# Kernel optimization log

Measured on AMD Instinct MI355X. Metric: run time of the kernel, lower is better.

## Reference

```python
import jax, jax.numpy as jnp
import numpy as np

DIM = 1024
HID = 2048
E = 8
K = 2
EPS = 1e-9


def setup_inputs() -> dict:
    key = jax.random.key(0)
    ks = jax.random.split(key, 6)
    scale = 0.02
    return {
        "x": jax.random.normal(ks[0], (4, 2048, DIM), jnp.float32),
        "gate_w": jax.random.normal(ks[1], (DIM, E), jnp.float32) * scale,
        "gate_b": jnp.zeros((E,), jnp.float32),
        # stacked expert weights: leading dim = expert index
        "w1": jax.random.normal(ks[2], (E, DIM, HID), jnp.float32) * scale,
        "b1": jnp.zeros((E, HID), jnp.float32),
        "w2": jax.random.normal(ks[3], (E, DIM, HID), jnp.float32) * scale,
        "b2": jnp.zeros((E, HID), jnp.float32),
        "w3": jax.random.normal(ks[4], (E, HID, DIM), jnp.float32) * scale,
        "b3": jnp.zeros((E, DIM), jnp.float32),
    }


def reference(x, gate_w, gate_b, w1, b1, w2, b2, w3, b3):
    # x: (b, s, d)
    logits = x @ gate_w + gate_b                      # (b, s, E)
    scores = jax.nn.softmax(logits, axis=-1)
    topk_scores, topk_idx = jax.lax.top_k(scores, K)  # (b, s, K)

    usage = scores.mean(axis=(0, 1))                  # (E,)
    load_balance_loss = jnp.sum(usage * jnp.log(usage + EPS))

    # per-expert combine weight: score if expert in top-k else 0  -> (b, s, E)
    onehot = jax.nn.one_hot(topk_idx, E, dtype=x.dtype)            # (b, s, K, E)
    combine = jnp.sum(topk_scores[..., None] * onehot, axis=2)     # (b, s, E)

    out = jnp.zeros_like(x)
    for e in range(E):  # small fixed loop over experts
        gate = jax.nn.sigmoid(x @ w2[e] + b2[e])      # (b, s, H)
        h = (x @ w1[e] + b1[e]) * gate                # SwiGLU hidden
        out = out + combine[..., e:e + 1] * (h @ w3[e] + b3[e])
    return out, load_balance_loss
```

## Files before the change

kernel.cpp:

```cpp
#include <hip/hip_runtime.h>
#include <hip/hip_bf16.h>
#include <math.h>

#define N_TOK 8192
#define DIM   1024
#define HID   2048
#define NE    8
#define NT1   16
#define NT2   32
#define NB1   16
#define NB2   4
#define MAXT  72
#define PANEL1_SH ((size_t)(128 * 256 * 8))
#define PANEL3_SH ((size_t)(256 * 256 * 8))
#define XBLK_SH   ((size_t)(128 * 128 * 8))
#define HBLK_SH   ((size_t)(256 * 128 * 8))

typedef __attribute__((ext_vector_type(8))) short short8;
typedef __attribute__((ext_vector_type(4))) float f32x4;
typedef unsigned short us;

__device__ __forceinline__ us f2bf(float f) {
    unsigned int u = __builtin_bit_cast(unsigned int, f);
    unsigned int r = (u + 0x7fffu + ((u >> 16) & 1u)) >> 16;
    return (us)r;
}

__device__ __forceinline__ void gl_lds16(const us* g, us* l) {
    __builtin_amdgcn_global_load_lds(
        (const __attribute__((address_space(1))) void*)g,
        (__attribute__((address_space(3))) void*)l, 16, 0, 0);
}

#define VMW4 asm volatile("s_waitcnt vmcnt(4)" ::: "memory")
#define VMW0 asm volatile("s_waitcnt vmcnt(0)" ::: "memory")
#define BARM asm volatile("s_barrier" ::: "memory")
#define PRIO1 __builtin_amdgcn_s_setprio(1)
#define PRIO0 __builtin_amdgcn_s_setprio(0)

__global__ __launch_bounds__(256) void gate_compute(
    const float* __restrict__ x, const float* __restrict__ gw, const float* __restrict__ gb,
    int* __restrict__ sel, float2* __restrict__ wpair, float* __restrict__ usage_part)
{
    const int lane = threadIdx.x & 63;
    const int tok = blockIdx.x * 4 + (threadIdx.x >> 6);

    __shared__ float su[NE];
    if (threadIdx.x < NE) su[threadIdx.x] = 0.f;
    __syncthreads();

    float acc[NE];
#pragma unroll
    for (int e = 0; e < NE; e++) acc[e] = 0.f;

    const float* xr = x + (size_t)tok * DIM;
    for (int d = lane; d < DIM; d += 64) {
        float xv = xr[d];
        const float4* g4 = (const float4*)(gw + (size_t)d * NE);
        float4 ga = g4[0], gc = g4[1];
        acc[0] = fmaf(xv, ga.x, acc[0]);
        acc[1] = fmaf(xv, ga.y, acc[1]);
        acc[2] = fmaf(xv, ga.z, acc[2]);
        acc[3] = fmaf(xv, ga.w, acc[3]);
        acc[4] = fmaf(xv, gc.x, acc[4]);
        acc[5] = fmaf(xv, gc.y, acc[5]);
        acc[6] = fmaf(xv, gc.z, acc[6]);
        acc[7] = fmaf(xv, gc.w, acc[7]);
    }
#pragma unroll
    for (int e = 0; e < NE; e++) {
#pragma unroll
        for (int off = 32; off > 0; off >>= 1)
            acc[e] += __shfl_xor(acc[e], off);
    }

    if (lane == 0) {
        float lg[NE], p[NE];
        float mx = -1e30f;
#pragma unroll
        for (int e = 0; e < NE; e++) { lg[e] = acc[e] + gb[e]; mx = fmaxf(mx, lg[e]); }
        float s = 0.f;
#pragma unroll
        for (int e = 0; e < NE; e++) { p[e] = __expf(lg[e] - mx); s += p[e]; }
        float inv = 1.f / s;
#pragma unroll
        for (int e = 0; e < NE; e++) p[e] *= inv;
#pragma unroll
        for (int e = 0; e < NE; e++) atomicAdd(&su[e], p[e]);

        int e1 = 0; float v1 = p[0];
#pragma unroll
        for (int e = 1; e < NE; e++) if (p[e] > v1) { v1 = p[e]; e1 = e; }
        int e2 = -1; float v2 = -1e30f;
#pragma unroll
        for (int e = 0; e < NE; e++) if (e != e1 && p[e] > v2) { v2 = p[e]; e2 = e; }

        sel[tok] = e1 | (e2 << 4);
        wpair[tok] = make_float2(v1, v2);
    }
    __syncthreads();
    if (threadIdx.x < NE) usage_part[blockIdx.x * NE + threadIdx.x] = su[threadIdx.x];
}

__global__ __launch_bounds__(256) void scan_kernel(
    const int* __restrict__ sel, const float2* __restrict__ wpair,
    int* __restrict__ counts, int* __restrict__ lists, float* __restrict__ wlist)
{
    const int e = blockIdx.x;
    const int t = threadIdx.x;
    const int base_tok = t * 32;

    unsigned selm = 0, km = 0;
#pragma unroll
    for (int i = 0; i < 32; i++) {
        int s = sel[base_tok + i];
        int e1 = s & 15, e2 = (s >> 4) & 15;
        if (e1 == e) selm |= (1u << i);
        else if (e2 == e) { selm |= (1u << i); km |= (1u << i); }
    }
    const int myc = __popc(selm);

    __shared__ int tot[256];
    tot[t] = myc;
    __syncthreads();
#pragma unroll
    for (int d = 1; d < 256; d <<= 1) {
        int v = (t >= d) ? tot[t - d] : 0;
        __syncthreads();
        tot[t] += v;
        __syncthreads();
    }
    int pos = tot[t] - myc;
    if (t == 255) counts[e] = tot[255];

    for (int i = 0; i < 32; i++) {
        if (selm & (1u << i)) {
            int tok = base_tok + i;
            int k = (km >> i) & 1;
            lists[e * N_TOK + pos] = tok * 2 + k;
            float2 wp = wpair[tok];
            wlist[e * N_TOK + pos] = k ? wp.y : wp.x;
            pos++;
        }
    }
}

__global__ __launch_bounds__(256) void usage_reduce(
    const float* __restrict__ part, float* __restrict__ usage)
{
    const int t = threadIdx.x;
    const int e = t & 7, chunk = t >> 3;
    float s = 0.f;
    for (int b = chunk; b < 2048; b += 32) s += part[b * NE + e];
    __shared__ float red[256];
    red[t] = s;
    __syncthreads();
#pragma unroll
    for (int step = 128; step >= 8; step >>= 1) {
        if (t < step) red[t] += red[t + step];
        __syncthreads();
    }
    if (t < NE) usage[t] = red[t];
}

__global__ void loss_kernel(const float* __restrict__ usage, float* __restrict__ out_loss)
{
    if (threadIdx.x == 0) {
        float l = 0.f;
        for (int e = 0; e < NE; e++) {
            float u = usage[e] / (float)N_TOK;
            l += u * logf(u + 1e-9f);
        }
        *out_loss = l;
    }
}

__global__ void prefix_kernel(const int* __restrict__ counts,
                              int* __restrict__ base_exact, int* __restrict__ ntiles,
                              int* __restrict__ tmap_e, int* __restrict__ tmap_m0)
{
    if (threadIdx.x == 0) {
        int bx = 0, nt = 0;
        for (int e = 0; e < NE; e++) {
            base_exact[e] = bx;
            for (int m0 = 0; m0 < counts[e]; m0 += 256) {
                tmap_e[nt] = e; tmap_m0[nt] = m0; nt++;
            }
            bx += counts[e];
        }
        ntiles[0] = nt;
    }
}

__global__ __launch_bounds__(256) void inv_kernel(
    const int* __restrict__ counts, const int* __restrict__ lists,
    const int* __restrict__ base_exact, int* __restrict__ inv)
{
    const int e = blockIdx.y;
    const int idx = blockIdx.x * 256 + threadIdx.x;
    if (idx < counts[e]) inv[lists[e * N_TOK + idx]] = base_exact[e] + idx;
}

__global__ __launch_bounds__(256) void xgather_kernel(
    const float* __restrict__ x,
    const int* __restrict__ counts, const int* __restrict__ lists,
    const int* __restrict__ base_exact,
    us* __restrict__ Xg)
{
    __shared__ int toks[128];
    __shared__ int bexs[NE], cnts[NE];
    const int t = threadIdx.x;
    if (t < NE) { bexs[t] = base_exact[t]; cnts[t] = counts[t]; }
    __syncthreads();
    if (t < 128) {
        int gpos = blockIdx.x * 128 + t;
        int e = 0;
#pragma unroll
        for (int k = 1; k < NE; k++) if (gpos >= bexs[k]) e = k;
        int idx = gpos - bexs[e];
        int tok = (idx < cnts[e]) ? (lists[e * N_TOK + idx] >> 1) : 0;
        toks[t] = tok;
    }
    __syncthreads();

    us* op = Xg + (size_t)blockIdx.x * XBLK_SH;
    const int rr = t & 127;
    const int ch = t >> 7;
    const int tok = toks[rr];
#pragma unroll
    for (int it = 0; it < 64; it++) {
        int c = it * 2 + ch;
        const float4* src = (const float4*)(x + (size_t)tok * DIM + c * 8);
        float4 a = src[0], b = src[1];
        short8 v;
        v[0] = (short)f2bf(a.x); v[1] = (short)f2bf(a.y);
        v[2] = (short)f2bf(a.z); v[3] = (short)f2bf(a.w);
        v[4] = (short)f2bf(b.x); v[5] = (short)f2bf(b.y);
        v[6] = (short)f2bf(b.z); v[7] = (short)f2bf(b.w);
        *(short8*)(op + (size_t)(c * 128 + rr) * 8) = v;
    }
}

__global__ __launch_bounds__(256) void wswz12_kernel(
    const float* __restrict__ w1, const float* __restrict__ w2, us* __restrict__ out)
{
    const int e = blockIdx.z, nbx = blockIdx.y, gs = blockIdx.x;
    us* op = out + ((size_t)e * NB1 + nbx) * PANEL1_SH + (size_t)gs * 8 * 256 * 8;
    const float* w1e = w1 + (size_t)e * DIM * HID;
    const float* w2e = w2 + (size_t)e * DIM * HID;
    const int t = threadIdx.x;
#pragma unroll
    for (int it = 0; it < 8; it++) {
        int idx = it * 256 + t;
        int g = idx >> 8, row = idx & 255;
        int col = nbx * 128 + (row & 127);
        const float* src = (row < 128 ? w1e : w2e) + (size_t)((gs * 8 + g) * 8) * HID + col;
        short8 v;
#pragma unroll
        for (int s = 0; s < 8; s++) v[s] = (short)f2bf(src[(size_t)s * HID]);
        *(short8*)(op + (size_t)idx * 8) = v;
    }
}

__global__ __launch_bounds__(256) void wswz3_kernel(
    const float* __restrict__ w3, us* __restrict__ out)
{
    const int e = blockIdx.z, nbx = blockIdx.y, gs = blockIdx.x;
    us* op = out + ((size_t)e * NB2 + nbx) * PANEL3_SH + (size_t)gs * 8 * 256 * 8;
    const float* w3e = w3 + (size_t)e * HID * DIM;
    const int t = threadIdx.x;
#pragma unroll
    for (int it = 0; it < 8; it++) {
        int idx = it * 256 + t;
        int g = idx >> 8, row = idx & 255;
        int col = nbx * 256 + row;
        const float* src = w3e + (size_t)((gs * 8 + g) * 8) * DIM + col;
        short8 v;
#pragma unroll
        for (int s = 0; s < 8; s++) v[s] = (short)f2bf(src[(size_t)s * DIM]);
        *(short8*)(op + (size_t)idx * 8) = v;
    }
}

#define ABUF(b) ((us*)(SM + (b)*32768))
#define BBUF(b) ((us*)(SM + 65536 + (b)*32768))

#define AF_READ(b, h) do {                                               \
    _Pragma("unroll")                                                    \
    for (int mi = 0; mi < 8; mi++)                                       \
        af[mi] = *(const short8*)(ABUF(b) + ((h)*1024 + kc*256 + Mw + mi*16 + fr)*8); \
} while (0)
#define BF_READ4(b, h) do {                                              \
    _Pragma("unroll")                                                    \
    for (int j = 0; j < 4; j++)                                          \
        bfv[j] = *(const short8*)(BBUF(b) + ((h)*1024 + kc*256 + Nw + j*16 + fr)*8); \
} while (0)
#define CLUST4 do {                                                      \
    PRIO1;                                                               \
    _Pragma("unroll")                                                    \
    for (int j = 0; j < 4; j++) {                                        \
        _Pragma("unroll")                                                \
        for (int mi = 0; mi < 8; mi++)                                   \
            acc[mi][j] = __builtin_amdgcn_mfma_f32_16x16x32_bf16(        \
                af[mi], bfv[j], acc[mi][j], 0, 0, 0);                    \
    }                                                                    \
    PRIO0;                                                               \
} while (0)

__global__ __launch_bounds__(512, 2) void ffn1_mfma_kernel(
    const us* __restrict__ Xg, const us* __restrict__ W12sw,
    const float* __restrict__ b1, const float* __restrict__ b2,
    const int* __restrict__ counts, const int* __restrict__ base_exact,
    const int* __restrict__ ntiles, const int* __restrict__ tmap_e, const int* __restrict__ tmap_m0,
    us* __restrict__ Hsw)
{
    const int hw = blockIdx.x;
    const int ix = hw >> 3;
    const int nbx = ((hw & 7) << 1) | (ix & 1);
    const int by  = ix >> 1;
    if (by >= ntiles[0]) return;
    const int e  = tmap_e[by];
    const int m0 = tmap_m0[by];
    const int cnt = counts[e];
    const int bex = base_exact[e];

    __shared__ __align__(16) unsigned char SM[132096];

    const int t = threadIdx.x;
    const int lane = t & 63, wv = t >> 6;
    const int wr = wv >> 2, wc = wv & 3;
    const int Mw = wr * 128, Nw = wc * 64;
    const int fr = lane & 15, kc = lane >> 4;

    float bb[4];
    {
        const float* bsrc = (wc < 2) ? b1 : b2;
#pragma unroll
        for (int ni = 0; ni < 4; ni++)
            bb[ni] = bsrc[e * HID + nbx * 128 + (wc & 1) * 64 + ni * 16 + fr];
    }
    __syncthreads();

    const int c0 = wv * 128 + lane;
    const int c1 = c0 + 64;
    const int RA0 = min(bex + m0 + (c0 & 255), N_TOK * 2 - 1);
    const int RA1 = min(bex + m0 + (c1 & 255), N_TOK * 2 - 1);
    const us* ApA = Xg + (size_t)(RA0 >> 7) * XBLK_SH + (size_t)(c0 >> 8) * 1024 + (RA0 & 127) * 8;
    const us* ApB = Xg + (size_t)(RA1 >> 7) * XBLK_SH + (size_t)(c1 >> 8) * 1024 + (RA1 & 127) * 8;
    const us* Wp = W12sw + ((size_t)e * NB1 + nbx) * PANEL1_SH;
    const int dbase = wv * 128 * 8;

    f32x4 acc[8][4];
    const f32x4 fz = {0.f, 0.f, 0.f, 0.f};
#pragma unroll
    for (int i = 0; i < 8; i++)
#pragma unroll
        for (int j = 0; j < 4; j++) acc[i][j] = fz;

    #define STAGE_A(b, tile, h) do {                                             \
        gl_lds16(ApA + (size_t)((tile)*8 + (h)*4) * 1024, ABUF(b) + ((h)*1024)*8 + dbase); \
        gl_lds16(ApB + (size_t)((tile)*8 + (h)*4) * 1024, ABUF(b) + ((h)*1024 + 64)*8 + dbase); \
    } while (0)
    #define STAGE_B(b, tile, h) do {                                             \
        const us* s_ = Wp + ((size_t)(tile)*2048 + (h)*1024) * 8;                \
        gl_lds16(s_ + (size_t)c0 * 8, BBUF(b) + ((h)*1024)*8 + dbase);           \
        gl_lds16(s_ + (size_t)c1 * 8, BBUF(b) + ((h)*1024 + 64)*8 + dbase);      \
    } while (0)

    short8 af[8], bfv[4];

    STAGE_A(0, 0, 0); STAGE_B(0, 0, 0); STAGE_A(0, 0, 1); STAGE_B(0, 0, 1);
    VMW4; BARM;

    for (int tl = 0; tl < NT1; ++tl) {
        const int b = tl & 1, nb = b ^ 1;
        const bool more = (tl + 1 < NT1);
        AF_READ(b, 0); BF_READ4(b, 0);
        if (more) { STAGE_A(nb, tl + 1, 0); STAGE_B(nb, tl + 1, 0); VMW4; } else { VMW0; }
        BARM; CLUST4; BARM;
        AF_READ(b, 1); BF_READ4(b, 1);
        if (more) { STAGE_A(nb, tl + 1, 1); STAGE_B(nb, tl + 1, 1); VMW4; }
        BARM; CLUST4; BARM;
    }
    #undef STAGE_A
    #undef STAGE_B

    float* G = (float*)SM;
    if (wc >= 2) {
        const int cp = wc - 2;
#pragma unroll
        for (int ni = 0; ni < 4; ni++) {
            int c2 = cp * 64 + ni * 16 + fr;
#pragma unroll
            for (int mi = 0; mi < 8; mi++) {
#pragma unroll
                for (int j = 0; j < 4; j++) {
                    int m = mi * 16 + kc * 4 + j;
                    float g = 1.f / (1.f + __expf(-(acc[mi][ni][j] + bb[ni])));
                    G[(wr * 128 + c2) * 129 + m] = g;
                }
            }
        }
    }
    __syncthreads();
    if (wc < 2) {
#pragma unroll
        for (int ni = 0; ni < 4; ni++) {
            int c2 = wc * 64 + ni * 16 + fr;
            int ch = nbx * 128 + c2;
            size_t cb = (size_t)(ch >> 3) * 128 * 8 + (ch & 7);
#pragma unroll
            for (int mi = 0; mi < 8; mi++) {
#pragma unroll
                for (int j = 0; j < 4; j++) {
                    int m = mi * 16 + kc * 4 + j;
                    int rl = wr * 128 + m;
                    if (m0 + rl >= cnt) continue;
                    float h = (acc[mi][ni][j] + bb[ni]) * G[(wr * 128 + c2) * 129 + m];
                    int R = bex + m0 + rl;
                    Hsw[(size_t)(R >> 7) * HBLK_SH + cb + (size_t)(R & 127) * 8] = f2bf(h);
                }
            }
        }
    }
}

__global__ __launch_bounds__(512, 2) void ffn2_mfma_kernel(
    const us* __restrict__ Hsw, const us* __restrict__ W3sw, const float* __restrict__ b3,
    const int* __restrict__ counts, const int* __restrict__ base_exact,
    const int* __restrict__ ntiles, const int* __restrict__ tmap_e, const int* __restrict__ tmap_m0,
    const float* __restrict__ wts,
    float* __restrict__ P, int pan0)
{
    const int hw = blockIdx.x;
    const int xcd = hw & 7;
    const int ix = hw >> 3;
    const int pn = xcd >> 2;
    const int by = (ix << 2) | (xcd & 3);
    if (by >= ntiles[0]) return;
    const int e  = tmap_e[by];
    const int m0 = tmap_m0[by];
    const int cnt = counts[e];
    const int bex = base_exact[e];
    const int nbx = pan0 + pn;

    __shared__ __align__(16) unsigned char SM[132096];
    float* rowwt = (float*)(SM + 131072);

    const int t = threadIdx.x;
    if (t < 256) {
        int idx = m0 + t;
        rowwt[t] = (idx < cnt) ? wts[e * N_TOK + idx] : 0.f;
    }

    const int lane = t & 63, wv = t >> 6;
    const int wr = wv >> 2, wc = wv & 3;
    const int Mw = wr * 128, Nw = wc * 64;
    const int fr = lane & 15, kc = lane >> 4;

    float bb3[4];
#pragma unroll
    for (int ni = 0; ni < 4; ni++)
        bb3[ni] = b3[e * DIM + nbx * 256 + wc * 64 + ni * 16 + fr];
    __syncthreads();

    const int c0 = wv * 128 + lane;
    const int c1 = c0 + 64;
    const int RA0 = min(bex + m0 + (c0 & 255), N_TOK * 2 - 1);
    const int RA1 = min(bex + m0 + (c1 & 255), N_TOK * 2 - 1);
    const us* HpA = Hsw + (size_t)(RA0 >> 7) * HBLK_SH + (size_t)(c0 >> 8) * 1024 + (RA0 & 127) * 8;
    const us* HpB = Hsw + (size_t)(RA1 >> 7) * HBLK_SH + (size_t)(c1 >> 8) * 1024 + (RA1 & 127) * 8;
    const us* Wp = W3sw + ((size_t)e * NB2 + nbx) * PANEL3_SH;
    const int dbase = wv * 128 * 8;

    f32x4 acc[8][4];
    const f32x4 fz = {0.f, 0.f, 0.f, 0.f};
#pragma unroll
    for (int i = 0; i < 8; i++)
#pragma unroll
        for (int j = 0; j < 4; j++) acc[i][j] = fz;

    #define STAGE_A2(b, tile, h) do {                                            \
        gl_lds16(HpA + (size_t)((tile)*8 + (h)*4) * 1024, ABUF(b) + ((h)*1024)*8 + dbase); \
        gl_lds16(HpB + (size_t)((tile)*8 + (h)*4) * 1024, ABUF(b) + ((h)*1024 + 64)*8 + dbase); \
    } while (0)
    #define STAGE_B2(b, tile, h) do {                                            \
        const us* s_ = Wp + ((size_t)(tile)*2048 + (h)*1024) * 8;                \
        gl_lds16(s_ + (size_t)c0 * 8, BBUF(b) + ((h)*1024)*8 + dbase);           \
        gl_lds16(s_ + (size_t)c1 * 8, BBUF(b) + ((h)*1024 + 64)*8 + dbase);      \
    } while (0)

    short8 af[8], bfv[4];

    STAGE_A2(0, 0, 0); STAGE_B2(0, 0, 0); STAGE_A2(0, 0, 1); STAGE_B2(0, 0, 1);
    VMW4; BARM;

    for (int tl = 0; tl < NT2; ++tl) {
        const int b = tl & 1, nb = b ^ 1;
        const bool more = (tl + 1 < NT2);
        AF_READ(b, 0); BF_READ4(b, 0);
        if (more) { STAGE_A2(nb, tl + 1, 0); STAGE_B2(nb, tl + 1, 0); VMW4; } else { VMW0; }
        BARM; CLUST4; BARM;
        AF_READ(b, 1); BF_READ4(b, 1);
        if (more) { STAGE_A2(nb, tl + 1, 1); STAGE_B2(nb, tl + 1, 1); VMW4; }
        BARM; CLUST4; BARM;
    }
    #undef STAGE_A2
    #undef STAGE_B2

#pragma unroll
    for (int ni = 0; ni < 4; ni++) {
        int cp = pn * 256 + wc * 64 + ni * 16 + fr;
#pragma unroll
        for (int mi = 0; mi < 8; mi++) {
#pragma unroll
            for (int j = 0; j < 4; j++) {
                int rl = wr * 128 + mi * 16 + kc * 4 + j;
                if (m0 + rl >= cnt) continue;
                float v = (acc[mi][ni][j] + bb3[ni]) * rowwt[rl];
                P[(size_t)(bex + m0 + rl) * 512 + cp] = v;
            }
        }
    }
}

__global__ __launch_bounds__(256) void combine_kernel(
    const float* __restrict__ P, const int* __restrict__ inv,
    float* __restrict__ out, int colbase)
{
    int gid = blockIdx.x * 256 + threadIdx.x;
    int tok = gid >> 7;
    int c4 = (gid & 127) * 4;
    const float4 a = *(const float4*)(P + (size_t)inv[tok * 2] * 512 + c4);
    const float4 b = *(const float4*)(P + (size_t)inv[tok * 2 + 1] * 512 + c4);
    float4 r = make_float4(a.x + b.x, a.y + b.y, a.z + b.z, a.w + b.w);
    *(float4*)(out + (size_t)tok * DIM + colbase + c4) = r;
}

extern "C" void kernel_launch(void* const* d_in, const int* in_sizes, int n_in,
                              void* d_out, int out_size, void* d_ws, size_t ws_size,
                              hipStream_t stream) {
    (void)in_sizes; (void)n_in; (void)out_size; (void)ws_size;
    const float* x      = (const float*)d_in[0];
    const float* gate_w = (const float*)d_in[1];
    const float* gate_b = (const float*)d_in[2];
    const float* w1     = (const float*)d_in[3];
    const float* b1     = (const float*)d_in[4];
    const float* w2     = (const float*)d_in[5];
    const float* b2     = (const float*)d_in[6];
    const float* w3     = (const float*)d_in[7];
    const float* b3     = (const float*)d_in[8];
    float* out = (float*)d_out;

    char* ws = (char*)d_ws;
    float* usage      = (float*)ws;
    int*   counts     = (int*)(ws + 32);
    int*   base_exact = (int*)(ws + 64);
    int*   ntiles     = (int*)(ws + 96);
    int*   tmap_e     = (int*)(ws + 128);
    int*   tmap_m0    = (int*)(ws + 640);
    int*   lists      = (int*)(ws + 4096);
    float* wts        = (float*)(ws + 4096 + (size_t)NE * N_TOK * 4);
    int*   inv        = (int*)(ws + 4096 + (size_t)2 * NE * N_TOK * 4);
    int*   sel        = (int*)(ws + 4096 + 576 * 1024);
    float2* wpair     = (float2*)(ws + 4096 + 608 * 1024);
    float* usage_part = (float*)(ws + 4096 + 672 * 1024);
    us* Hsw   = (us*)(ws + (1ull  << 20));
    us* W12sw = (us*)(ws + (65ull << 20));
    us* W3sw  = W12sw;
    float* P  = (float*)(ws + (97ull << 20));
    us* Xg    = (us*)d_out;

    gate_compute<<<N_TOK / 4, 256, 0, stream>>>(x, gate_w, gate_b, sel, wpair, usage_part);
    scan_kernel<<<NE, 256, 0, stream>>>(sel, wpair, counts, lists, wts);
    usage_reduce<<<1, 256, 0, stream>>>(usage_part, usage);
    prefix_kernel<<<1, 64, 0, stream>>>(counts, base_exact, ntiles, tmap_e, tmap_m0);
    {
        dim3 gI(N_TOK / 256, NE);
        inv_kernel<<<gI, 256, 0, stream>>>(counts, lists, base_exact, inv);
    }
    xgather_kernel<<<N_TOK * 2 / 128, 256, 0, stream>>>(x, counts, lists, base_exact, Xg);

    dim3 gW12(16, NB1, NE);
    wswz12_kernel<<<gW12, 256, 0, stream>>>(w1, w2, W12sw);

    ffn1_mfma_kernel<<<NB1 * MAXT, 512, 0, stream>>>(Xg, W12sw, b1, b2, counts, base_exact,
                                                     ntiles, tmap_e, tmap_m0, Hsw);

    loss_kernel<<<1, 64, 0, stream>>>(usage, out + (size_t)N_TOK * DIM);

    dim3 gW3(32, NB2, NE);
    wswz3_kernel<<<gW3, 256, 0, stream>>>(w3, W3sw);

    ffn2_mfma_kernel<<<2 * MAXT, 512, 0, stream>>>(Hsw, W3sw, b3, counts, base_exact,
                                                   ntiles, tmap_e, tmap_m0, wts, P, 0);
    combine_kernel<<<N_TOK * 128 / 256, 256, 0, stream>>>(P, inv, out, 0);
    ffn2_mfma_kernel<<<2 * MAXT, 512, 0, stream>>>(Hsw, W3sw, b3, counts, base_exact,
                                                   ntiles, tmap_e, tmap_m0, wts, P, 2);
    combine_kernel<<<N_TOK * 128 / 256, 256, 0, stream>>>(P, inv, out, 512);
}
```

Baseline: 495.8 us.

## Store expert outputs as bf16 and fuse the two ffn2 column passes into one launch

The partial expert-output buffer changes from fp32 to bf16, so its width goes from half of DIM to full DIM within the same workspace footprint. That lets ffn2 run over all four column panels in a single launch, and the combine kernel runs once instead of twice. This removes two launches and halves the bytes written and read for the intermediate results. The cost is an extra bf16 rounding of each weighted expert output before the two top-k contributions are summed, which adds some precision loss.

```diff
diff --git a/kernel.cpp b/kernel.cpp
--- a/kernel.cpp
+++ b/kernel.cpp
@@ -24,6 +24,11 @@
     unsigned int u = __builtin_bit_cast(unsigned int, f);
     unsigned int r = (u + 0x7fffu + ((u >> 16) & 1u)) >> 16;
     return (us)r;
+}
+
+__device__ __forceinline__ float bf2f(us v) {
+    unsigned int u = ((unsigned int)v) << 16;
+    return __builtin_bit_cast(float, u);
 }
 
 __device__ __forceinline__ void gl_lds16(const us* g, us* l) {
@@ -430,19 +435,18 @@
     const int* __restrict__ counts, const int* __restrict__ base_exact,
     const int* __restrict__ ntiles, const int* __restrict__ tmap_e, const int* __restrict__ tmap_m0,
     const float* __restrict__ wts,
-    float* __restrict__ P, int pan0)
+    us* __restrict__ Pb)
 {
     const int hw = blockIdx.x;
     const int xcd = hw & 7;
     const int ix = hw >> 3;
-    const int pn = xcd >> 2;
-    const int by = (ix << 2) | (xcd & 3);
+    const int nbx = xcd & 3;
+    const int by = (ix << 1) | (xcd >> 2);
     if (by >= ntiles[0]) return;
     const int e  = tmap_e[by];
     const int m0 = tmap_m0[by];
     const int cnt = counts[e];
     const int bex = base_exact[e];
-    const int nbx = pan0 + pn;
 
     __shared__ __align__(16) unsigned char SM[132096];
     float* rowwt = (float*)(SM + 131072);
@@ -510,7 +514,7 @@
 
 #pragma unroll
     for (int ni = 0; ni < 4; ni++) {
-        int cp = pn * 256 + wc * 64 + ni * 16 + fr;
+        int col = nbx * 256 + wc * 64 + ni * 16 + fr;
 #pragma unroll
         for (int mi = 0; mi < 8; mi++) {
 #pragma unroll
@@ -518,23 +522,33 @@
                 int rl = wr * 128 + mi * 16 + kc * 4 + j;
                 if (m0 + rl >= cnt) continue;
                 float v = (acc[mi][ni][j] + bb3[ni]) * rowwt[rl];
-                P[(size_t)(bex + m0 + rl) * 512 + cp] = v;
+                Pb[(size_t)(bex + m0 + rl) * DIM + col] = f2bf(v);
             }
         }
     }
 }
 
 __global__ __launch_bounds__(256) void combine_kernel(
-    const float* __restrict__ P, const int* __restrict__ inv,
-    float* __restrict__ out, int colbase)
+    const us* __restrict__ Pb, const int* __restrict__ inv,
+    float* __restrict__ out)
 {
     int gid = blockIdx.x * 256 + threadIdx.x;
     int tok = gid >> 7;
-    int c4 = (gid & 127) * 4;
-    const float4 a = *(const float4*)(P + (size_t)inv[tok * 2] * 512 + c4);
-    const float4 b = *(const float4*)(P + (size_t)inv[tok * 2 + 1] * 512 + c4);
-    float4 r = make_float4(a.x + b.x, a.y + b.y, a.z + b.z, a.w + b.w);
-    *(float4*)(out + (size_t)tok * DIM + colbase + c4) = r;
+    int c8 = (gid & 127) * 8;
+    const short8 a = *(const short8*)(Pb + (size_t)inv[tok * 2] * DIM + c8);
+    const short8 b = *(const short8*)(Pb + (size_t)inv[tok * 2 + 1] * DIM + c8);
+    float4 r0, r1;
+    r0.x = bf2f((us)a[0]) + bf2f((us)b[0]);
+    r0.y = bf2f((us)a[1]) + bf2f((us)b[1]);
+    r0.z = bf2f((us)a[2]) + bf2f((us)b[2]);
+    r0.w = bf2f((us)a[3]) + bf2f((us)b[3]);
+    r1.x = bf2f((us)a[4]) + bf2f((us)b[4]);
+    r1.y = bf2f((us)a[5]) + bf2f((us)b[5]);
+    r1.z = bf2f((us)a[6]) + bf2f((us)b[6]);
+    r1.w = bf2f((us)a[7]) + bf2f((us)b[7]);
+    float* o = out + (size_t)tok * DIM + c8;
+    *(float4*)o = r0;
+    *(float4*)(o + 4) = r1;
 }
 
 extern "C" void kernel_launch(void* const* d_in, const int* in_sizes, int n_in,
@@ -568,7 +582,7 @@
     us* Hsw   = (us*)(ws + (1ull  << 20));
     us* W12sw = (us*)(ws + (65ull << 20));
     us* W3sw  = W12sw;
-    float* P  = (float*)(ws + (97ull << 20));
+    us* Pb    = (us*)(ws + (97ull << 20));
     us* Xg    = (us*)d_out;
 
     gate_compute<<<N_TOK / 4, 256, 0, stream>>>(x, gate_w, gate_b, sel, wpair, usage_part);
@@ -592,10 +606,7 @@
     dim3 gW3(32, NB2, NE);
     wswz3_kernel<<<gW3, 256, 0, stream>>>(w3, W3sw);
 
-    ffn2_mfma_kernel<<<2 * MAXT, 512, 0, stream>>>(Hsw, W3sw, b3, counts, base_exact,
-                                                   ntiles, tmap_e, tmap_m0, wts, P, 0);
-    combine_kernel<<<N_TOK * 128 / 256, 256, 0, stream>>>(P, inv, out, 0);
-    ffn2_mfma_kernel<<<2 * MAXT, 512, 0, stream>>>(Hsw, W3sw, b3, counts, base_exact,
-                                                   ntiles, tmap_e, tmap_m0, wts, P, 2);
-    combine_kernel<<<N_TOK * 128 / 256, 256, 0, stream>>>(P, inv, out, 512);
-}
+    ffn2_mfma_kernel<<<4 * MAXT, 512, 0, stream>>>(Hsw, W3sw, b3, counts, base_exact,
+                                                   ntiles, tmap_e, tmap_m0, wts, Pb);
+    combine_kernel<<<N_TOK * 128 / 256, 256, 0, stream>>>(Pb, inv, out);
+}
```

After: 502.2 us. Within noise of the previous version (+1.3%).
